# Kernel tuning notes

Hardware: AMD Instinct MI355X
Metric: run time of the kernel (lower is better)

The kernel has to match this reference:

```python
import jax, jax.numpy as jnp
import numpy as np

N_EMBED = 1024
NUM_EXPERTS = 8
TOP_K = 2
N_ROUTERS = 5
SEQ = 2048


def setup_inputs() -> dict:
    key = jax.random.key(0)
    ks = jax.random.split(key, 10)
    d, E, R, H = N_EMBED, NUM_EXPERTS, N_ROUTERS, 4 * N_EMBED
    x = jax.random.normal(ks[0], (R, SEQ, d), dtype=jnp.float32)
    moe = jnp.arange(R, dtype=jnp.int64) if jax.config.jax_enable_x64 else jnp.arange(R, dtype=jnp.int32)
    s = 0.02
    Wr = s * jax.random.normal(ks[1], (R, d, E), dtype=jnp.float32)
    br = jnp.zeros((R, E), dtype=jnp.float32)
    Wn = s * jax.random.normal(ks[2], (R, d, E), dtype=jnp.float32)
    bn = jnp.zeros((R, E), dtype=jnp.float32)
    W1 = s * jax.random.normal(ks[3], (E, d, H), dtype=jnp.float32)
    b1 = jnp.zeros((E, H), dtype=jnp.float32)
    W2 = s * jax.random.normal(ks[4], (E, H, d), dtype=jnp.float32)
    b2 = jnp.zeros((E, d), dtype=jnp.float32)
    return {"x": x, "moe": moe, "Wr": Wr, "br": br, "Wn": Wn, "bn": bn,
            "W1": W1, "b1": b1, "W2": W2, "b2": b2}


def reference(x, moe, Wr, br, Wn, bn, W1, b1, W2, b2):
    # Per-batch router selection: router[moe[b]] applied to x[b]
    logits = jnp.einsum('btd,bde->bte', x, Wr[moe]) + br[moe][:, None, :]
    noise_logits = jnp.einsum('btd,bde->bte', x, Wn[moe]) + bn[moe][:, None, :]
    eps = jax.random.normal(jax.random.key(42), logits.shape, logits.dtype)
    noisy = logits + eps * jax.nn.softplus(noise_logits)  # [B,T,E]

    topv, topi = jax.lax.top_k(noisy, TOP_K)  # [B,T,K]
    E = noisy.shape[-1]
    # selected[b,t,e] = e in top-k indices; equivalent to scatter of top-k logits into -inf
    selected = jnp.any(topi[..., None] == jnp.arange(E), axis=-2)  # [B,T,E]
    sparse = jnp.where(selected, noisy, -jnp.inf)
    gating = jax.nn.softmax(sparse, axis=-1)  # zero for non-selected experts

    B, T, d = x.shape
    flat_x = x.reshape(-1, d)            # [B*T, d]
    flat_g = gating.reshape(-1, E)       # [B*T, E]
    out = jnp.zeros_like(flat_x)
    for e in range(E):  # fixed small set of experts
        h = jax.nn.relu(flat_x @ W1[e] + b1[e])   # [B*T, 4d]
        o = h @ W2[e] + b2[e]                      # [B*T, d]
        out = out + o * flat_g[:, e:e + 1]         # gating is 0 off top-k
    final_output = out.reshape(B, T, d)
    return final_output, topi
```

## Files before the change

### kernel.cpp

```cpp
#include <hip/hip_runtime.h>
#include <hip/hip_bf16.h>
#include <cstdint>

#define NTOK   10240
#define DIM    1024
#define NEXP   8
#define HDIM   4096
#define NSLOT  20480
#define MAXSLOT 21504
#define MAXTILES 168

typedef __attribute__((ext_vector_type(8))) __bf16 bf16x8;
typedef __attribute__((ext_vector_type(4))) float  f32x4;

__device__ __forceinline__ unsigned short f2bf(float f){
  uint32_t u = __float_as_uint(f);
  uint32_t r = (u + 0x7fffu + ((u >> 16) & 1u)) >> 16;
  return (unsigned short)r;
}
__device__ __forceinline__ float bf2f(unsigned short u){
  return __uint_as_float(((uint32_t)u) << 16);
}

__device__ __forceinline__ void gl_lds16(const void* g, void* l){
  __builtin_amdgcn_global_load_lds(
      (const __attribute__((address_space(1))) void*)g,
      (__attribute__((address_space(3))) void*)l, 16, 0, 0);
}

__device__ __forceinline__ int swz_wid(){
  int nwg = (int)(gridDim.x * gridDim.y);
  int h   = (int)(blockIdx.y * gridDim.x + blockIdx.x);
  int q = nwg >> 3, r = nwg & 7;
  int xcd = h & 7, idx = h >> 3;
  return (xcd < r ? xcd*(q+1) : r*(q+1) + (xcd-r)*q) + idx;
}

__device__ __forceinline__ uint32_t rotl32(uint32_t x, int n){ return (x << n) | (x >> (32 - n)); }

__device__ __forceinline__ uint32_t threefry_xor(uint32_t k0, uint32_t k1, uint32_t x0, uint32_t x1){
  uint32_t ks2 = k0 ^ k1 ^ 0x1BD11BDAu;
  uint32_t ks[3] = {k0, k1, ks2};
  x0 += ks[0]; x1 += ks[1];
  const int rA[4] = {13,15,26,6};
  const int rB[4] = {17,29,16,24};
  #pragma unroll
  for (int i = 0; i < 5; ++i){
    #pragma unroll
    for (int j = 0; j < 4; ++j){
      int rot = (i & 1) ? rB[j] : rA[j];
      x0 += x1; x1 = rotl32(x1, rot); x1 ^= x0;
    }
    x0 += ks[(i+1)%3];
    x1 += ks[(i+2)%3] + (uint32_t)(i+1);
  }
  return x0 ^ x1;
}

__device__ __forceinline__ float erfinv_f32(float x){
  float w = -log1pf(-x*x);
  float p;
  if (w < 5.0f){
    w -= 2.5f;
    p = 2.81022636e-08f;
    p = fmaf(p, w, 3.43273939e-07f);
    p = fmaf(p, w, -3.5233877e-06f);
    p = fmaf(p, w, -4.39150654e-06f);
    p = fmaf(p, w, 0.00021858087f);
    p = fmaf(p, w, -0.00125372503f);
    p = fmaf(p, w, -0.00417768164f);
    p = fmaf(p, w, 0.246640727f);
    p = fmaf(p, w, 1.50140941f);
  } else {
    w = sqrtf(w) - 3.0f;
    p = -0.000200214257f;
    p = fmaf(p, w, 0.000100950558f);
    p = fmaf(p, w, 0.00134934322f);
    p = fmaf(p, w, -0.00367342844f);
    p = fmaf(p, w, 0.00573950773f);
    p = fmaf(p, w, -0.0076224613f);
    p = fmaf(p, w, 0.00943887047f);
    p = fmaf(p, w, 1.00167406f);
    p = fmaf(p, w, 2.83297682f);
  }
  return p * x;
}

__global__ void transpose_cvt_kernel(const float* __restrict__ src, unsigned short* __restrict__ dst,
                                     int R_, int C_){
  __shared__ float tile[32][33];
  int z = blockIdx.z;
  const float* s = src + (size_t)z * R_ * C_;
  unsigned short* d = dst + (size_t)z * R_ * C_;
  int c0 = blockIdx.x * 32, r0 = blockIdx.y * 32;
  #pragma unroll
  for (int i = threadIdx.y; i < 32; i += 8)
    tile[i][threadIdx.x] = s[(size_t)(r0 + i) * C_ + c0 + threadIdx.x];
  __syncthreads();
  #pragma unroll
  for (int i = threadIdx.y; i < 32; i += 8)
    d[(size_t)(c0 + i) * R_ + r0 + threadIdx.x] = f2bf(tile[threadIdx.x][i]);
}

__global__ __launch_bounds__(256) void route_kernel(
    const float* __restrict__ x, const int* __restrict__ moe,
    const float* __restrict__ Wr, const float* __restrict__ br,
    const float* __restrict__ Wn, const float* __restrict__ bn,
    float* __restrict__ topi_out, int* __restrict__ te, float* __restrict__ tgv,
    unsigned short* __restrict__ xb)
{
  const int wv = threadIdx.x >> 6, lane = threadIdx.x & 63;
  const int tok = (int)blockIdx.x * 4 + wv;
  const int b = tok >> 11;
  const int r = moe[b];
  const float4* xr  = (const float4*)(x + (size_t)tok * DIM);
  const float4* wrp = (const float4*)(Wr + (size_t)r * DIM * NEXP);
  const float4* wnp = (const float4*)(Wn + (size_t)r * DIM * NEXP);
  ushort4* xbrow = (ushort4*)(xb + (size_t)tok * DIM);

  float lg[8], nl[8];
  #pragma unroll
  for (int e = 0; e < 8; ++e){ lg[e] = 0.f; nl[e] = 0.f; }

  #pragma unroll
  for (int it = 0; it < 4; ++it){
    int d4 = it*64 + lane;
    float4 xv = xr[d4];
    ushort4 o;
    o.x = f2bf(xv.x); o.y = f2bf(xv.y); o.z = f2bf(xv.z); o.w = f2bf(xv.w);
    xbrow[d4] = o;
    #pragma unroll
    for (int j = 0; j < 4; ++j){
      float xs = (j==0) ? xv.x : (j==1) ? xv.y : (j==2) ? xv.z : xv.w;
      float4 w0 = wrp[d4*8 + j*2], w1 = wrp[d4*8 + j*2 + 1];
      float4 n0 = wnp[d4*8 + j*2], n1 = wnp[d4*8 + j*2 + 1];
      lg[0] = fmaf(xs, w0.x, lg[0]); lg[1] = fmaf(xs, w0.y, lg[1]);
      lg[2] = fmaf(xs, w0.z, lg[2]); lg[3] = fmaf(xs, w0.w, lg[3]);
      lg[4] = fmaf(xs, w1.x, lg[4]); lg[5] = fmaf(xs, w1.y, lg[5]);
      lg[6] = fmaf(xs, w1.z, lg[6]); lg[7] = fmaf(xs, w1.w, lg[7]);
      nl[0] = fmaf(xs, n0.x, nl[0]); nl[1] = fmaf(xs, n0.y, nl[1]);
      nl[2] = fmaf(xs, n0.z, nl[2]); nl[3] = fmaf(xs, n0.w, nl[3]);
      nl[4] = fmaf(xs, n1.x, nl[4]); nl[5] = fmaf(xs, n1.y, nl[5]);
      nl[6] = fmaf(xs, n1.z, nl[6]); nl[7] = fmaf(xs, n1.w, nl[7]);
    }
  }

  #pragma unroll
  for (int e = 0; e < 8; ++e){
    #pragma unroll
    for (int s = 32; s >= 1; s >>= 1){
      lg[e] += __shfl_xor(lg[e], s, 64);
      nl[e] += __shfl_xor(nl[e], s, 64);
    }
  }

  int el = lane & 7;
  float mylg = lg[0], mynl = nl[0];
  #pragma unroll
  for (int e = 1; e < 8; ++e){
    if (el == e){ mylg = lg[e]; mynl = nl[e]; }
  }
  float logit = mylg + br[r*NEXP + el];
  float nlg   = mynl + bn[r*NEXP + el];
  uint32_t idx  = (uint32_t)(tok*NEXP + el);
  uint32_t bits = threefry_xor(0u, 42u, 0u, idx);
  float u01 = __uint_as_float((bits >> 9) | 0x3f800000u) - 1.0f;
  const float lo = -0.99999994f;
  float uu  = fmaxf(lo, u01 * 2.0f + lo);
  float eps = 1.41421356237f * erfinv_f32(uu);
  float ax = fabsf(nlg);
  float sp = fmaxf(nlg, 0.0f) + log1pf(expf(-ax));
  float noisy = logit + eps * sp;

  float nv[8];
  #pragma unroll
  for (int e = 0; e < 8; ++e) nv[e] = __shfl(noisy, e, 64);

  if (lane == 0){
    int i0 = 0; float v0 = nv[0];
    int i1 = -1; float v1 = -3.4e38f;
    #pragma unroll
    for (int e = 1; e < 8; ++e){
      float v = nv[e];
      if (v > v0){ v1 = v0; i1 = i0; v0 = v; i0 = e; }
      else if (v > v1){ v1 = v; i1 = e; }
    }
    float t = expf(v1 - v0);
    float s = 1.0f + t;
    topi_out[tok*2 + 0] = (float)i0;
    topi_out[tok*2 + 1] = (float)i1;
    te[tok*2 + 0] = i0; te[tok*2 + 1] = i1;
    tgv[tok*2 + 0] = 1.0f / s; tgv[tok*2 + 1] = t / s;
  }
}

__global__ __launch_bounds__(256) void count_kernel(const int* __restrict__ te,
                                                    unsigned* __restrict__ counts){
  int id = blockIdx.x * 256 + threadIdx.x;
  int e = te[id];
  int lane = threadIdx.x & 63;
  #pragma unroll
  for (int ee = 0; ee < 8; ++ee){
    unsigned long long m = __ballot(e == ee);
    if (m && lane == (__ffsll((unsigned long long)m) - 1))
      atomicAdd(&counts[ee], (unsigned)__popcll(m));
  }
}

__global__ void tables_kernel(unsigned* __restrict__ hdr, int* __restrict__ tile_expert,
                              int* __restrict__ rows)
{
  __shared__ unsigned offs_s[NEXP+1];
  __shared__ unsigned cnt_s[NEXP];
  if (threadIdx.x == 0){
    unsigned o = 0, tt = 0;
    for (int e = 0; e < NEXP; ++e){
      unsigned c = hdr[e];
      cnt_s[e] = c;
      offs_s[e] = o;
      hdr[8 + e] = o;
      unsigned nt = (c + 127u) / 128u;
      for (unsigned k = 0; k < nt; ++k) tile_expert[tt++] = e;
      o += nt * 128u;
    }
    offs_s[NEXP] = o;
    hdr[16] = tt;
  }
  __syncthreads();
  for (int e = 0; e < NEXP; ++e){
    unsigned start = offs_s[e] + cnt_s[e];
    unsigned end   = offs_s[e+1];
    for (unsigned i = start + threadIdx.x; i < end; i += blockDim.x)
      rows[i] = 0;
  }
}

__global__ __launch_bounds__(256) void scatter_kernel(const int* __restrict__ te,
                               unsigned* __restrict__ cursor, int* __restrict__ rows,
                               int* __restrict__ slot_idx)
{
  int id = blockIdx.x * 256 + threadIdx.x;
  int tok = id >> 1;
  int e = te[id];
  int lane = threadIdx.x & 63;
  unsigned long long below = ((unsigned long long)1 << lane) - 1ull;
  unsigned myslot = 0;
  #pragma unroll
  for (int ee = 0; ee < 8; ++ee){
    unsigned long long m = __ballot(e == ee);
    if (e == ee){
      int leader = __ffsll((unsigned long long)m) - 1;
      unsigned base = 0;
      if (lane == leader) base = atomicAdd(&cursor[ee], (unsigned)__popcll(m));
      base = __shfl(base, leader, 64);
      myslot = base + (unsigned)__popcll(m & below);
    }
  }
  rows[myslot] = tok;
  slot_idx[id] = (int)myslot;
}

__global__ __launch_bounds__(512) void gemm1_kernel(
    const unsigned short* __restrict__ Xb,
    const unsigned short* __restrict__ W1t,
    const float* __restrict__ b1,
    const int* __restrict__ rows, const int* __restrict__ tile_expert,
    const unsigned* __restrict__ hdr,
    unsigned short* __restrict__ H)
{
  const int w  = swz_wid();
  const int xn = w % (int)gridDim.x;
  const int tg = w / (int)gridDim.x;
  if (tg >= (int)hdr[16]) return;
  const int e  = tile_expert[tg];
  const int n0 = xn * 128;
  const int tid = threadIdx.x;
  const int wid = tid >> 6, lane = tid & 63;
  const int wr = wid >> 2, wc = wid & 3;
  const int l8 = lane & 7, ld8 = lane >> 3;
  const int srcsw = (l8 ^ ld8) * 8;

  __shared__ __align__(16) unsigned short As[128][64];
  __shared__ __align__(16) unsigned short Bs[128][64];

  const unsigned short* aSrc[2];
  const unsigned short* bSrc[2];
  #pragma unroll
  for (int i = 0; i < 2; ++i){
    int rrow = wid*16 + i*8 + ld8;
    int tokr = rows[tg*128 + rrow];
    aSrc[i] = Xb  + (size_t)tokr * DIM + srcsw;
    bSrc[i] = W1t + ((size_t)e * HDIM + n0 + rrow) * DIM + srcsw;
  }

  f32x4 acc[4][2];
  #pragma unroll
  for (int m = 0; m < 4; ++m)
    #pragma unroll
    for (int n = 0; n < 2; ++n) acc[m][n] = (f32x4)(0.0f);

  const int l15 = lane & 15, lq = lane >> 4, l7 = lane & 7;

  for (int kk = 0; kk < DIM; kk += 64){
    #pragma unroll
    for (int i = 0; i < 2; ++i){
      gl_lds16(aSrc[i] + kk, &As[wid*16 + i*8][0]);
      gl_lds16(bSrc[i] + kk, &Bs[wid*16 + i*8][0]);
    }
    __syncthreads();
    #pragma unroll
    for (int ks = 0; ks < 2; ++ks){
      const int ch = ((ks*4 + lq) ^ l7) * 8;
      bf16x8 af[4], bfv[2];
      #pragma unroll
      for (int m = 0; m < 4; ++m)
        af[m] = *reinterpret_cast<const bf16x8*>(&As[wr*64 + m*16 + l15][ch]);
      #pragma unroll
      for (int n = 0; n < 2; ++n)
        bfv[n] = *reinterpret_cast<const bf16x8*>(&Bs[wc*32 + n*16 + l15][ch]);
      #pragma unroll
      for (int m = 0; m < 4; ++m)
        #pragma unroll
        for (int n = 0; n < 2; ++n)
          acc[m][n] = __builtin_amdgcn_mfma_f32_16x16x32_bf16(af[m], bfv[n], acc[m][n], 0, 0, 0);
    }
    __syncthreads();
  }

  const int hrow0 = tg * 128;
  #pragma unroll
  for (int n = 0; n < 2; ++n){
    int c = n0 + wc*32 + n*16 + l15;
    float bv = b1[(size_t)e * HDIM + c];
    #pragma unroll
    for (int m = 0; m < 4; ++m){
      #pragma unroll
      for (int j = 0; j < 4; ++j){
        int rloc = wr*64 + m*16 + lq*4 + j;
        float v = fmaxf(acc[m][n][j] + bv, 0.0f);
        H[(size_t)(hrow0 + rloc) * HDIM + c] = f2bf(v);
      }
    }
  }
}

__global__ __launch_bounds__(512) void gemm2_kernel(
    const unsigned short* __restrict__ H,
    const unsigned short* __restrict__ W2t,
    const float* __restrict__ b2,
    const int* __restrict__ tile_expert, const unsigned* __restrict__ hdr,
    unsigned short* __restrict__ O2)
{
  const int w  = swz_wid();
  const int xn = w % (int)gridDim.x;
  const int tg = w / (int)gridDim.x;
  if (tg >= (int)hdr[16]) return;
  const int e  = tile_expert[tg];
  const int n0 = xn * 128;
  const int tid = threadIdx.x;
  const int wid = tid >> 6, lane = tid & 63;
  const int wr = wid >> 2, wc = wid & 3;
  const int l8 = lane & 7, ld8 = lane >> 3;
  const int srcsw = (l8 ^ ld8) * 8;

  __shared__ __align__(16) unsigned short As[128][64];
  __shared__ __align__(16) unsigned short Bs[128][64];

  const unsigned short* aSrc[2];
  const unsigned short* bSrc[2];
  #pragma unroll
  for (int i = 0; i < 2; ++i){
    int rrow = wid*16 + i*8 + ld8;
    aSrc[i] = H   + (size_t)(tg*128 + rrow) * HDIM + srcsw;
    bSrc[i] = W2t + ((size_t)e * DIM + n0 + rrow) * HDIM + srcsw;
  }

  f32x4 acc[4][2];
  #pragma unroll
  for (int m = 0; m < 4; ++m)
    #pragma unroll
    for (int n = 0; n < 2; ++n) acc[m][n] = (f32x4)(0.0f);

  const int l15 = lane & 15, lq = lane >> 4, l7 = lane & 7;

  for (int kk = 0; kk < HDIM; kk += 64){
    #pragma unroll
    for (int i = 0; i < 2; ++i){
      gl_lds16(aSrc[i] + kk, &As[wid*16 + i*8][0]);
      gl_lds16(bSrc[i] + kk, &Bs[wid*16 + i*8][0]);
    }
    __syncthreads();
    #pragma unroll
    for (int ks = 0; ks < 2; ++ks){
      const int ch = ((ks*4 + lq) ^ l7) * 8;
      bf16x8 af[4], bfv[2];
      #pragma unroll
      for (int m = 0; m < 4; ++m)
        af[m] = *reinterpret_cast<const bf16x8*>(&As[wr*64 + m*16 + l15][ch]);
      #pragma unroll
      for (int n = 0; n < 2; ++n)
        bfv[n] = *reinterpret_cast<const bf16x8*>(&Bs[wc*32 + n*16 + l15][ch]);
      #pragma unroll
      for (int m = 0; m < 4; ++m)
        #pragma unroll
        for (int n = 0; n < 2; ++n)
          acc[m][n] = __builtin_amdgcn_mfma_f32_16x16x32_bf16(af[m], bfv[n], acc[m][n], 0, 0, 0);
    }
    __syncthreads();
  }

  #pragma unroll
  for (int n = 0; n < 2; ++n){
    int c = n0 + wc*32 + n*16 + l15;
    float bv = b2[(size_t)e * DIM + c];
    #pragma unroll
    for (int m = 0; m < 4; ++m){
      #pragma unroll
      for (int j = 0; j < 4; ++j){
        int rloc = wr*64 + m*16 + lq*4 + j;
        O2[(size_t)(tg*128 + rloc) * DIM + c] = f2bf(acc[m][n][j] + bv);
      }
    }
  }
}

__global__ __launch_bounds__(256) void combine_kernel(
    const unsigned short* __restrict__ O2, const int* __restrict__ slot_idx,
    const float* __restrict__ tgv, float* __restrict__ out)
{
  int tok = blockIdx.x;
  int d4  = threadIdx.x;
  int s0 = slot_idx[tok*2], s1 = slot_idx[tok*2 + 1];
  float g0 = tgv[tok*2], g1 = tgv[tok*2 + 1];
  ushort4 a = ((const ushort4*)(O2 + (size_t)s0 * DIM))[d4];
  ushort4 b = ((const ushort4*)(O2 + (size_t)s1 * DIM))[d4];
  float4 o;
  o.x = g0*bf2f(a.x) + g1*bf2f(b.x);
  o.y = g0*bf2f(a.y) + g1*bf2f(b.y);
  o.z = g0*bf2f(a.z) + g1*bf2f(b.z);
  o.w = g0*bf2f(a.w) + g1*bf2f(b.w);
  ((float4*)(out + (size_t)tok * DIM))[d4] = o;
}

extern "C" void kernel_launch(void* const* d_in, const int* in_sizes, int n_in,
                              void* d_out, int out_size, void* d_ws, size_t ws_size,
                              hipStream_t stream)
{
  const float* x  = (const float*)d_in[0];
  const int*   moe= (const int*)  d_in[1];
  const float* Wr = (const float*)d_in[2];
  const float* br = (const float*)d_in[3];
  const float* Wn = (const float*)d_in[4];
  const float* bn = (const float*)d_in[5];
  const float* W1 = (const float*)d_in[6];
  const float* b1 = (const float*)d_in[7];
  const float* W2 = (const float*)d_in[8];
  const float* b2 = (const float*)d_in[9];
  float* out = (float*)d_out;
  float* topi_out = out + (size_t)NTOK * DIM;

  char* ws = (char*)d_ws;
  size_t off = 0;
  auto take = [&](size_t bytes)->char*{
    char* p = ws + off;
    off = (off + bytes + 255) & ~(size_t)255;
    return p;
  };
  unsigned* hdr        = (unsigned*)take(128);
  int*      tile_exp   = (int*)     take(MAXTILES * 4);
  int*      rows       = (int*)     take(MAXSLOT * 4);
  int*      te         = (int*)     take(NSLOT * 4);
  float*    tgv        = (float*)   take(NSLOT * 4);
  int*      slot_idx   = (int*)     take(NSLOT * 4);
  unsigned short* xb   = (unsigned short*)take((size_t)NTOK * DIM * 2);
  unsigned short* W1t  = (unsigned short*)take((size_t)NEXP * HDIM * DIM * 2);
  unsigned short* W2t  = (unsigned short*)take((size_t)NEXP * DIM * HDIM * 2);
  unsigned short* O2   = (unsigned short*)take((size_t)MAXSLOT * DIM * 2);

  size_t avail = (ws_size > off) ? (ws_size - off) : 0;
  size_t maxrows = avail / ((size_t)HDIM * 2);
  int tpc = (int)(maxrows / 128);
  if (tpc > MAXTILES) tpc = MAXTILES;
  if (tpc < 1) tpc = 1;
  unsigned short* H = (unsigned short*)take((size_t)tpc * 128 * HDIM * 2);

  hipMemsetAsync(hdr, 0, 128, stream);

  dim3 tb(32, 8);
  transpose_cvt_kernel<<<dim3(HDIM/32, DIM/32, NEXP), tb, 0, stream>>>(W1, W1t, DIM, HDIM);
  transpose_cvt_kernel<<<dim3(DIM/32, HDIM/32, NEXP), tb, 0, stream>>>(W2, W2t, HDIM, DIM);
  route_kernel<<<NTOK/4, 256, 0, stream>>>(x, moe, Wr, br, Wn, bn, topi_out, te, tgv, xb);
  count_kernel<<<NSLOT/256, 256, 0, stream>>>(te, hdr);
  tables_kernel<<<1, 64, 0, stream>>>(hdr, tile_exp, rows);
  scatter_kernel<<<NSLOT/256, 256, 0, stream>>>(te, hdr + 8, rows, slot_idx);

  if (tpc >= MAXTILES){
    gemm1_kernel<<<dim3(HDIM/128, MAXTILES), 512, 0, stream>>>(xb, W1t, b1, rows, tile_exp, hdr, H);
    gemm2_kernel<<<dim3(DIM/128,  MAXTILES), 512, 0, stream>>>(H, W2t, b2, tile_exp, hdr, O2);
  } else {
    for (int t0 = 0; t0 < MAXTILES; t0 += tpc){
      int nt = (tpc < MAXTILES - t0) ? tpc : (MAXTILES - t0);
      unsigned short* Hoff = H - (size_t)t0 * 128 * HDIM;
      gemm1_kernel<<<dim3(HDIM/128, nt), 512, 0, stream>>>(xb, W1t, b1, rows + t0*128,
                                                           tile_exp + t0, hdr, Hoff);
      gemm2_kernel<<<dim3(DIM/128,  nt), 512, 0, stream>>>(Hoff, W2t, b2, tile_exp + t0, hdr,
                                                           O2 + (size_t)t0*128*DIM);
    }
  }
  combine_kernel<<<NTOK, 256, 0, stream>>>(O2, slot_idx, tgv, out);
}
```

Measured before the change: 742.5 us.

## Double-buffer LDS tiles in both expert GEMMs to overlap loads with MFMA

Both grouped GEMM kernels now keep two LDS buffers for the A and B tiles. They issue the global-to-LDS copies for the next K step before computing on the current one, using explicit vmcnt waits and s_barrier fences instead of __syncthreads. MFMA sections are wrapped in s_setprio to favour the math waves. This hides global load latency behind compute, at the cost of doubling LDS use (64KB per block), which may lower occupancy.

```diff
diff --git a/kernel.cpp b/kernel.cpp
--- a/kernel.cpp
+++ b/kernel.cpp
@@ -279,9 +279,10 @@
   const int wr = wid >> 2, wc = wid & 3;
   const int l8 = lane & 7, ld8 = lane >> 3;
   const int srcsw = (l8 ^ ld8) * 8;
-
-  __shared__ __align__(16) unsigned short As[128][64];
-  __shared__ __align__(16) unsigned short Bs[128][64];
+  const int l15 = lane & 15, lq = lane >> 4, l7 = lane & 7;
+
+  __shared__ __align__(16) unsigned short As[2][128][64];
+  __shared__ __align__(16) unsigned short Bs[2][128][64];
 
   const unsigned short* aSrc[2];
   const unsigned short* bSrc[2];
@@ -299,32 +300,53 @@
     #pragma unroll
     for (int n = 0; n < 2; ++n) acc[m][n] = (f32x4)(0.0f);
 
-  const int l15 = lane & 15, lq = lane >> 4, l7 = lane & 7;
-
-  for (int kk = 0; kk < DIM; kk += 64){
+  auto stage = [&](int b, int kk){
     #pragma unroll
     for (int i = 0; i < 2; ++i){
-      gl_lds16(aSrc[i] + kk, &As[wid*16 + i*8][0]);
-      gl_lds16(bSrc[i] + kk, &Bs[wid*16 + i*8][0]);
-    }
-    __syncthreads();
+      gl_lds16(aSrc[i] + kk, &As[b][wid*16 + i*8][0]);
+      gl_lds16(bSrc[i] + kk, &Bs[b][wid*16 + i*8][0]);
+    }
+  };
+
+  stage(0, 0);
+  __builtin_amdgcn_sched_barrier(0);
+
+  const int NT = DIM / 64;
+  int cur = 0;
+  for (int t = 0; t < NT; ++t){
+    if (t + 1 < NT){
+      stage(cur ^ 1, (t + 1) * 64);
+      __builtin_amdgcn_sched_barrier(0);
+      asm volatile("s_waitcnt vmcnt(4)" ::: "memory");
+    } else {
+      asm volatile("s_waitcnt vmcnt(0)" ::: "memory");
+    }
+    __builtin_amdgcn_sched_barrier(0);
+    __builtin_amdgcn_s_barrier();
+    __builtin_amdgcn_sched_barrier(0);
+
     #pragma unroll
     for (int ks = 0; ks < 2; ++ks){
       const int ch = ((ks*4 + lq) ^ l7) * 8;
       bf16x8 af[4], bfv[2];
       #pragma unroll
       for (int m = 0; m < 4; ++m)
-        af[m] = *reinterpret_cast<const bf16x8*>(&As[wr*64 + m*16 + l15][ch]);
+        af[m] = *reinterpret_cast<const bf16x8*>(&As[cur][wr*64 + m*16 + l15][ch]);
       #pragma unroll
       for (int n = 0; n < 2; ++n)
-        bfv[n] = *reinterpret_cast<const bf16x8*>(&Bs[wc*32 + n*16 + l15][ch]);
+        bfv[n] = *reinterpret_cast<const bf16x8*>(&Bs[cur][wc*32 + n*16 + l15][ch]);
+      __builtin_amdgcn_s_setprio(1);
       #pragma unroll
       for (int m = 0; m < 4; ++m)
         #pragma unroll
         for (int n = 0; n < 2; ++n)
           acc[m][n] = __builtin_amdgcn_mfma_f32_16x16x32_bf16(af[m], bfv[n], acc[m][n], 0, 0, 0);
-    }
-    __syncthreads();
+      __builtin_amdgcn_s_setprio(0);
+    }
+    __builtin_amdgcn_sched_barrier(0);
+    __builtin_amdgcn_s_barrier();
+    __builtin_amdgcn_sched_barrier(0);
+    cur ^= 1;
   }
 
   const int hrow0 = tg * 128;
@@ -362,9 +384,10 @@
   const int wr = wid >> 2, wc = wid & 3;
   const int l8 = lane & 7, ld8 = lane >> 3;
   const int srcsw = (l8 ^ ld8) * 8;
-
-  __shared__ __align__(16) unsigned short As[128][64];
-  __shared__ __align__(16) unsigned short Bs[128][64];
+  const int l15 = lane & 15, lq = lane >> 4, l7 = lane & 7;
+
+  __shared__ __align__(16) unsigned short As[2][128][64];
+  __shared__ __align__(16) unsigned short Bs[2][128][64];
 
   const unsigned short* aSrc[2];
   const unsigned short* bSrc[2];
@@ -381,32 +404,53 @@
     #pragma unroll
     for (int n = 0; n < 2; ++n) acc[m][n] = (f32x4)(0.0f);
 
-  const int l15 = lane & 15, lq = lane >> 4, l7 = lane & 7;
-
-  for (int kk = 0; kk < HDIM; kk += 64){
+  auto stage = [&](int b, int kk){
     #pragma unroll
     for (int i = 0; i < 2; ++i){
-      gl_lds16(aSrc[i] + kk, &As[wid*16 + i*8][0]);
-      gl_lds16(bSrc[i] + kk, &Bs[wid*16 + i*8][0]);
-    }
-    __syncthreads();
+      gl_lds16(aSrc[i] + kk, &As[b][wid*16 + i*8][0]);
+      gl_lds16(bSrc[i] + kk, &Bs[b][wid*16 + i*8][0]);
+    }
+  };
+
+  stage(0, 0);
+  __builtin_amdgcn_sched_barrier(0);
+
+  const int NT = HDIM / 64;
+  int cur = 0;
+  for (int t = 0; t < NT; ++t){
+    if (t + 1 < NT){
+      stage(cur ^ 1, (t + 1) * 64);
+      __builtin_amdgcn_sched_barrier(0);
+      asm volatile("s_waitcnt vmcnt(4)" ::: "memory");
+    } else {
+      asm volatile("s_waitcnt vmcnt(0)" ::: "memory");
+    }
+    __builtin_amdgcn_sched_barrier(0);
+    __builtin_amdgcn_s_barrier();
+    __builtin_amdgcn_sched_barrier(0);
+
     #pragma unroll
     for (int ks = 0; ks < 2; ++ks){
       const int ch = ((ks*4 + lq) ^ l7) * 8;
       bf16x8 af[4], bfv[2];
       #pragma unroll
       for (int m = 0; m < 4; ++m)
-        af[m] = *reinterpret_cast<const bf16x8*>(&As[wr*64 + m*16 + l15][ch]);
+        af[m] = *reinterpret_cast<const bf16x8*>(&As[cur][wr*64 + m*16 + l15][ch]);
       #pragma unroll
       for (int n = 0; n < 2; ++n)
-        bfv[n] = *reinterpret_cast<const bf16x8*>(&Bs[wc*32 + n*16 + l15][ch]);
+        bfv[n] = *reinterpret_cast<const bf16x8*>(&Bs[cur][wc*32 + n*16 + l15][ch]);
+      __builtin_amdgcn_s_setprio(1);
       #pragma unroll
       for (int m = 0; m < 4; ++m)
         #pragma unroll
         for (int n = 0; n < 2; ++n)
           acc[m][n] = __builtin_amdgcn_mfma_f32_16x16x32_bf16(af[m], bfv[n], acc[m][n], 0, 0, 0);
-    }
-    __syncthreads();
+      __builtin_amdgcn_s_setprio(0);
+    }
+    __builtin_amdgcn_sched_barrier(0);
+    __builtin_amdgcn_s_barrier();
+    __builtin_amdgcn_sched_barrier(0);
+    cur ^= 1;
   }
 
   #pragma unroll
```

Result: no change. 735.5 us (-0.9%).
